# Performance work log

Measured on AMD Instinct MI355X. Metric: run time of the kernel, lower is better.

## Reference

```python
import jax, jax.numpy as jnp
import numpy as np

N_CELLS = 100000
IN_CH = 64
N_EDGES = 1280000


def setup_inputs() -> dict:
    key = jax.random.key(0)
    k1, k2, k3, k4, k5 = jax.random.split(key, 5)
    x_source = jax.random.normal(k1, (N_CELLS, IN_CH), dtype=jnp.float32)
    att_weight = jax.random.normal(k2, (2 * IN_CH,), dtype=jnp.float32)
    nbhd_values = jax.random.uniform(k3, (N_EDGES,), dtype=jnp.float32)
    target_index_i = jnp.sort(jax.random.randint(k4, (N_EDGES,), 0, N_CELLS))
    source_index_j = jax.random.randint(k5, (N_EDGES,), 0, N_CELLS)
    return {
        "x_source": x_source,
        "att_weight": att_weight,
        "nbhd_values": nbhd_values,
        "target_index_i": target_index_i,
        "source_index_j": source_index_j,
    }


def reference(x_source, att_weight, nbhd_values, target_index_i, source_index_j):
    # gather per-message endpoint features: [E, C] each
    x_src_msg = x_source[source_index_j]
    x_tgt_msg = x_source[target_index_i]  # x_target is None -> use x_source
    # attention: elu(cat([src, tgt]) @ w) -> [E]
    att = jax.nn.elu(
        jnp.concatenate([x_src_msg, x_tgt_msg], axis=1) @ att_weight
    )
    # modulate sparse neighborhood values by attention, scale messages
    vals = nbhd_values * att  # [E]
    x_message = vals[:, None] * x_src_msg  # [E, C]
    # scatter-sum into target cells: [N, C]
    return jax.ops.segment_sum(x_message, target_index_i, num_segments=N_CELLS)
```

## Files before the change

kernel.cpp:

```cpp
#include <hip/hip_runtime.h>

#define N_CELLS 100000
#define IN_CH 64
#define N_EDGES 1280000
#define NSEG 4
#define MAXW 4

__device__ __forceinline__ unsigned short f32_to_bf16(float f) {
    unsigned u = __float_as_uint(f);
    u += 0x7FFFu + ((u >> 16) & 1u);
    return (unsigned short)(u >> 16);
}
__device__ __forceinline__ float bf16_to_f32(unsigned short h) {
    return __uint_as_float((unsigned)h << 16);
}

#define SCORE_BLOCKS ((N_CELLS * 16 + 255) / 256)
#define ROWSTART_BLOCKS ((N_EDGES + 255) / 256)

__global__ void __launch_bounds__(256) prep_kernel(
    const float* __restrict__ x, const float* __restrict__ w,
    const int* __restrict__ tgt,
    float* __restrict__ s_src, float* __restrict__ s_tgt,
    unsigned short* __restrict__ xb, int* __restrict__ row_start,
    int n_cells, int n_edges) {
    if (blockIdx.x < SCORE_BLOCKS) {
        int gid  = blockIdx.x * 256 + threadIdx.x;
        int wave = gid >> 6;
        int lane = threadIdx.x & 63;
        int grp  = lane >> 4;
        int sub  = lane & 15;
        int cell = wave * 4 + grp;

        float4 xv = make_float4(0.f, 0.f, 0.f, 0.f);
        if (cell < n_cells)
            xv = *(const float4*)&x[(((unsigned)cell << 6) | ((unsigned)sub << 2))];
        if (xb && cell < n_cells) {
            ushort4 hb;
            hb.x = f32_to_bf16(xv.x); hb.y = f32_to_bf16(xv.y);
            hb.z = f32_to_bf16(xv.z); hb.w = f32_to_bf16(xv.w);
            *(ushort4*)&xb[(((unsigned)cell << 6) | ((unsigned)sub << 2))] = hb;
        }
        const float4* w4 = (const float4*)w;
        float4 wa = w4[sub];
        float4 wb = w4[16 + sub];
        float a = xv.x * wa.x + xv.y * wa.y + xv.z * wa.z + xv.w * wa.w;
        float b = xv.x * wb.x + xv.y * wb.y + xv.z * wb.z + xv.w * wb.w;
#pragma unroll
        for (int off = 8; off; off >>= 1) {
            a += __shfl_xor(a, off, 64);
            b += __shfl_xor(b, off, 64);
        }
        if (sub == 0 && cell < n_cells) {
            s_src[cell] = a;
            s_tgt[cell] = b;
        }
    } else {
        int e = (blockIdx.x - SCORE_BLOCKS) * 256 + threadIdx.x;
        if (e >= n_edges) return;
        int lane = threadIdx.x & 63;
        int t = tgt[e];
        int prev = __shfl_up(t, 1, 64);
        if (lane == 0) prev = (e == 0) ? -1 : tgt[e - 1];
        for (int c = prev + 1; c <= t; ++c) row_start[c] = e;
        if (e == n_edges - 1) {
            for (int c = t + 1; c <= n_cells; ++c) row_start[c] = n_edges;
        }
    }
}

__global__ void __launch_bounds__(256) agg_kernel_seg(
    const unsigned short* __restrict__ xb, const int* __restrict__ src,
    const float* __restrict__ nbhd,
    const float* __restrict__ s_src, const float* __restrict__ s_tgt,
    const int* __restrict__ row_start,
    float* __restrict__ out, int n_cells) {
    int gid  = blockIdx.x * blockDim.x + threadIdx.x;
    int lane = threadIdx.x & 63;
    int grp  = lane >> 4;
    int sub  = lane & 15;
    int cell = (gid >> 6) * 4 + grp;
    unsigned suboff = (unsigned)sub << 2;
    int gbase = grp << 4;

    int lo  = row_start[cell];
    int hi  = row_start[cell + 1];
    float sti = s_tgt[cell];
    int cnt  = hi - lo;
    int cntP = cnt > (MAXW * 16) ? (MAXW * 16) : cnt;

    const int q = (N_CELLS + NSEG - 1) / NSEG;

    int      jr[MAXW];
    float    vr[MAXW];
    unsigned bb[MAXW];

#pragma unroll
    for (int c = 0; c < MAXW; ++c) {
        int wcnt = cntP - (c << 4);
        wcnt = wcnt < 0 ? 0 : (wcnt > 16 ? 16 : wcnt);
        bool act = sub < wcnt;
        int j = 0; float v = 0.f;
        if (act) {
            int idx = lo + (c << 4) + sub;
            j = src[idx];
            float a = s_src[j] + sti;
            v = nbhd[idx] * (a > 0.f ? a : expm1f(a));
        }
        int b = act ? ((j >= 3 * q) ? 3 : (j >= 2 * q) ? 2 : (j >= q) ? 1 : 0) : 4;
        unsigned long long m0 = __ballot(b == 0);
        unsigned long long m1 = __ballot(b == 1);
        unsigned long long m2 = __ballot(b == 2);
        unsigned long long m3 = __ballot(b == 3);
        unsigned f0 = (unsigned)(m0 >> gbase) & 0xFFFFu;
        unsigned f1 = (unsigned)(m1 >> gbase) & 0xFFFFu;
        unsigned f2 = (unsigned)(m2 >> gbase) & 0xFFFFu;
        unsigned f3 = (unsigned)(m3 >> gbase) & 0xFFFFu;
        unsigned below = (1u << sub) - 1u;
        int c0 = __popc(f0), c1 = __popc(f1), c2 = __popc(f2), c3 = __popc(f3);
        int slot;
        if (b == 0)      slot = __popc(f0 & below);
        else if (b == 1) slot = c0 + __popc(f1 & below);
        else if (b == 2) slot = c0 + c1 + __popc(f2 & below);
        else if (b == 3) slot = c0 + c1 + c2 + __popc(f3 & below);
        else {
            unsigned f4 = ~(f0 | f1 | f2 | f3) & 0xFFFFu;
            slot = c0 + c1 + c2 + c3 + __popc(f4 & below);
        }
        int dst = (gbase + slot) << 2;
        jr[c] = __builtin_amdgcn_ds_permute(dst, j);
        vr[c] = __int_as_float(__builtin_amdgcn_ds_permute(dst, __float_as_int(v)));
        bb[c] = (unsigned)c0 | ((unsigned)(c0 + c1) << 5)
              | ((unsigned)(c0 + c1 + c2) << 10)
              | ((unsigned)(c0 + c1 + c2 + c3) << 15);
    }

    float4 acc = make_float4(0.f, 0.f, 0.f, 0.f);
#pragma unroll
    for (int s = 0; s < NSEG; ++s) {
#pragma unroll
        for (int c = 0; c < MAXW; ++c) {
            int t0 = (s == 0) ? 0 : (int)((bb[c] >> (5 * (s - 1))) & 31u);
            int t1 = (int)((bb[c] >> (5 * s)) & 31u);
            int t = t0;
            for (; t + 4 <= t1; t += 4) {
                int   j0 = __shfl(jr[c], gbase + t,     64);
                int   j1 = __shfl(jr[c], gbase + t + 1, 64);
                int   j2 = __shfl(jr[c], gbase + t + 2, 64);
                int   j3 = __shfl(jr[c], gbase + t + 3, 64);
                float v0 = __shfl(vr[c], gbase + t,     64);
                float v1 = __shfl(vr[c], gbase + t + 1, 64);
                float v2 = __shfl(vr[c], gbase + t + 2, 64);
                float v3 = __shfl(vr[c], gbase + t + 3, 64);
                ushort4 h0 = *(const ushort4*)&xb[(((unsigned)j0 << 6) | suboff)];
                ushort4 h1 = *(const ushort4*)&xb[(((unsigned)j1 << 6) | suboff)];
                ushort4 h2 = *(const ushort4*)&xb[(((unsigned)j2 << 6) | suboff)];
                ushort4 h3 = *(const ushort4*)&xb[(((unsigned)j3 << 6) | suboff)];
                acc.x = fmaf(v0, bf16_to_f32(h0.x), acc.x);
                acc.y = fmaf(v0, bf16_to_f32(h0.y), acc.y);
                acc.z = fmaf(v0, bf16_to_f32(h0.z), acc.z);
                acc.w = fmaf(v0, bf16_to_f32(h0.w), acc.w);
                acc.x = fmaf(v1, bf16_to_f32(h1.x), acc.x);
                acc.y = fmaf(v1, bf16_to_f32(h1.y), acc.y);
                acc.z = fmaf(v1, bf16_to_f32(h1.z), acc.z);
                acc.w = fmaf(v1, bf16_to_f32(h1.w), acc.w);
                acc.x = fmaf(v2, bf16_to_f32(h2.x), acc.x);
                acc.y = fmaf(v2, bf16_to_f32(h2.y), acc.y);
                acc.z = fmaf(v2, bf16_to_f32(h2.z), acc.z);
                acc.w = fmaf(v2, bf16_to_f32(h2.w), acc.w);
                acc.x = fmaf(v3, bf16_to_f32(h3.x), acc.x);
                acc.y = fmaf(v3, bf16_to_f32(h3.y), acc.y);
                acc.z = fmaf(v3, bf16_to_f32(h3.z), acc.z);
                acc.w = fmaf(v3, bf16_to_f32(h3.w), acc.w);
            }
            for (; t < t1; ++t) {
                int   jt = __shfl(jr[c], gbase + t, 64);
                float vt = __shfl(vr[c], gbase + t, 64);
                ushort4 h = *(const ushort4*)&xb[(((unsigned)jt << 6) | suboff)];
                acc.x = fmaf(vt, bf16_to_f32(h.x), acc.x);
                acc.y = fmaf(vt, bf16_to_f32(h.y), acc.y);
                acc.z = fmaf(vt, bf16_to_f32(h.z), acc.z);
                acc.w = fmaf(vt, bf16_to_f32(h.w), acc.w);
            }
        }
        if (s < NSEG - 1) __syncthreads();
    }

    for (int base = lo + MAXW * 16; base < hi; base += 16) {
        int cc = hi - base;
        if (cc > 16) cc = 16;
        int   j = 0;
        float v = 0.f;
        if (sub < cc) {
            j = src[base + sub];
            float a = s_src[j] + sti;
            v = nbhd[base + sub] * (a > 0.f ? a : expm1f(a));
        }
        for (int t = 0; t < cc; ++t) {
            int   jt = __shfl(j, gbase + t, 64);
            float vt = __shfl(v, gbase + t, 64);
            ushort4 h = *(const ushort4*)&xb[(((unsigned)jt << 6) | suboff)];
            acc.x = fmaf(vt, bf16_to_f32(h.x), acc.x);
            acc.y = fmaf(vt, bf16_to_f32(h.y), acc.y);
            acc.z = fmaf(vt, bf16_to_f32(h.z), acc.z);
            acc.w = fmaf(vt, bf16_to_f32(h.w), acc.w);
        }
    }

    *(float4*)&out[(((unsigned)cell << 6) | suboff)] = acc;
}

__global__ void __launch_bounds__(256) agg_kernel_f32(
    const float* __restrict__ x, const int* __restrict__ src,
    const float* __restrict__ nbhd,
    const float* __restrict__ s_src, const float* __restrict__ s_tgt,
    const int* __restrict__ row_start,
    float* __restrict__ out, int n_cells) {
    int gid  = blockIdx.x * blockDim.x + threadIdx.x;
    int lane = threadIdx.x & 63;
    int grp  = lane >> 4;
    int sub  = lane & 15;
    int cell = (gid >> 6) * 4 + grp;
    unsigned suboff = (unsigned)sub << 2;
    int gbase = grp << 4;

    int lo = 0, hi = 0;
    float sti = 0.f;
    if (cell < n_cells) {
        lo  = row_start[cell];
        hi  = row_start[cell + 1];
        sti = s_tgt[cell];
    }
    float4 acc = make_float4(0.f, 0.f, 0.f, 0.f);
    for (int base = lo; base < hi; base += 16) {
        int cc = hi - base;
        if (cc > 16) cc = 16;
        int   j = 0;
        float v = 0.f;
        if (sub < cc) {
            j = src[base + sub];
            float a = s_src[j] + sti;
            v = nbhd[base + sub] * (a > 0.f ? a : expm1f(a));
        }
        for (int t = 0; t < cc; ++t) {
            int   jt = __shfl(j, gbase + t, 64);
            float vt = __shfl(v, gbase + t, 64);
            float4 xt = *(const float4*)&x[(((unsigned)jt << 6) | suboff)];
            acc.x = fmaf(vt, xt.x, acc.x); acc.y = fmaf(vt, xt.y, acc.y);
            acc.z = fmaf(vt, xt.z, acc.z); acc.w = fmaf(vt, xt.w, acc.w);
        }
    }
    if (cell < n_cells)
        *(float4*)&out[(((unsigned)cell << 6) | suboff)] = acc;
}

extern "C" void kernel_launch(void* const* d_in, const int* in_sizes, int n_in,
                              void* d_out, int out_size, void* d_ws, size_t ws_size,
                              hipStream_t stream) {
    const float* x    = (const float*)d_in[0];
    const float* w    = (const float*)d_in[1];
    const float* nbhd = (const float*)d_in[2];
    const int*   tgt  = (const int*)d_in[3];
    const int*   src  = (const int*)d_in[4];
    float*       out  = (float*)d_out;

    float* s_src     = (float*)d_ws;
    float* s_tgt     = s_src + N_CELLS;
    int*   row_start = (int*)(s_tgt + N_CELLS);
    unsigned short* xb = (unsigned short*)(row_start + N_CELLS + 1);
    size_t need_bf16 = (size_t)(2 * N_CELLS + N_CELLS + 1) * 4 + (size_t)N_CELLS * IN_CH * 2;
    bool use_bf16 = ws_size >= need_bf16;

    if (use_bf16) {
        int blocks = SCORE_BLOCKS + ROWSTART_BLOCKS;
        prep_kernel<<<blocks, 256, 0, stream>>>(x, w, tgt, s_src, s_tgt, xb,
                                                row_start, N_CELLS, N_EDGES);
        int ablocks = (N_CELLS * 16) / 256;
        agg_kernel_seg<<<ablocks, 256, 0, stream>>>(xb, src, nbhd, s_src, s_tgt,
                                                    row_start, out, N_CELLS);
    } else {
        int blocks = SCORE_BLOCKS + ROWSTART_BLOCKS;
        prep_kernel<<<blocks, 256, 0, stream>>>(x, w, tgt, s_src, s_tgt,
                                                (unsigned short*)nullptr,
                                                row_start, N_CELLS, N_EDGES);
        int threads = 256;
        int ablocks = (N_CELLS * 16 + threads - 1) / threads;
        agg_kernel_f32<<<ablocks, threads, 0, stream>>>(x, src, nbhd, s_src, s_tgt,
                                                        row_start, out, N_CELLS);
    }
}
```

Measured before the change: 67.89 us.

## Precompute per-edge attention values in separate edge kernel, drop source-range bucketing

Splits the prep kernel into a score kernel and an edge kernel. The edge kernel computes each edge's elu-modulated weight once, stores it in a workspace array, and builds the row-start table. The aggregation kernel then only loads src and the precomputed value, with no s_src gather or expm1. It also drops the four-way source-range bucketing with ballots, permutes and block barriers in favour of a simple unrolled-by-8 gather loop. This adds a third launch, a dependency between score and edge kernels, and an extra write and read of the per-edge value array, and it gives up whatever locality the bucketing provided.

```diff
diff --git a/kernel.cpp b/kernel.cpp
--- a/kernel.cpp
+++ b/kernel.cpp
@@ -3,7 +3,6 @@
 #define N_CELLS 100000
 #define IN_CH 64
 #define N_EDGES 1280000
-#define NSEG 4
 #define MAXW 4
 
 __device__ __forceinline__ unsigned short f32_to_bf16(float f) {
@@ -15,67 +14,67 @@
     return __uint_as_float((unsigned)h << 16);
 }
 
-#define SCORE_BLOCKS ((N_CELLS * 16 + 255) / 256)
-#define ROWSTART_BLOCKS ((N_EDGES + 255) / 256)
-
-__global__ void __launch_bounds__(256) prep_kernel(
+__global__ void __launch_bounds__(256) score_kernel(
     const float* __restrict__ x, const float* __restrict__ w,
-    const int* __restrict__ tgt,
     float* __restrict__ s_src, float* __restrict__ s_tgt,
-    unsigned short* __restrict__ xb, int* __restrict__ row_start,
-    int n_cells, int n_edges) {
-    if (blockIdx.x < SCORE_BLOCKS) {
-        int gid  = blockIdx.x * 256 + threadIdx.x;
-        int wave = gid >> 6;
-        int lane = threadIdx.x & 63;
-        int grp  = lane >> 4;
-        int sub  = lane & 15;
-        int cell = wave * 4 + grp;
-
-        float4 xv = make_float4(0.f, 0.f, 0.f, 0.f);
-        if (cell < n_cells)
-            xv = *(const float4*)&x[(((unsigned)cell << 6) | ((unsigned)sub << 2))];
-        if (xb && cell < n_cells) {
-            ushort4 hb;
-            hb.x = f32_to_bf16(xv.x); hb.y = f32_to_bf16(xv.y);
-            hb.z = f32_to_bf16(xv.z); hb.w = f32_to_bf16(xv.w);
-            *(ushort4*)&xb[(((unsigned)cell << 6) | ((unsigned)sub << 2))] = hb;
-        }
-        const float4* w4 = (const float4*)w;
-        float4 wa = w4[sub];
-        float4 wb = w4[16 + sub];
-        float a = xv.x * wa.x + xv.y * wa.y + xv.z * wa.z + xv.w * wa.w;
-        float b = xv.x * wb.x + xv.y * wb.y + xv.z * wb.z + xv.w * wb.w;
-#pragma unroll
-        for (int off = 8; off; off >>= 1) {
-            a += __shfl_xor(a, off, 64);
-            b += __shfl_xor(b, off, 64);
-        }
-        if (sub == 0 && cell < n_cells) {
-            s_src[cell] = a;
-            s_tgt[cell] = b;
-        }
-    } else {
-        int e = (blockIdx.x - SCORE_BLOCKS) * 256 + threadIdx.x;
-        if (e >= n_edges) return;
-        int lane = threadIdx.x & 63;
-        int t = tgt[e];
-        int prev = __shfl_up(t, 1, 64);
-        if (lane == 0) prev = (e == 0) ? -1 : tgt[e - 1];
-        for (int c = prev + 1; c <= t; ++c) row_start[c] = e;
-        if (e == n_edges - 1) {
-            for (int c = t + 1; c <= n_cells; ++c) row_start[c] = n_edges;
-        }
-    }
-}
-
-__global__ void __launch_bounds__(256) agg_kernel_seg(
-    const unsigned short* __restrict__ xb, const int* __restrict__ src,
+    unsigned short* __restrict__ xb, int n_cells) {
+    int gid  = blockIdx.x * 256 + threadIdx.x;
+    int wave = gid >> 6;
+    int lane = threadIdx.x & 63;
+    int grp  = lane >> 4;
+    int sub  = lane & 15;
+    int cell = wave * 4 + grp;
+
+    float4 xv = make_float4(0.f, 0.f, 0.f, 0.f);
+    if (cell < n_cells)
+        xv = *(const float4*)&x[(((unsigned)cell << 6) | ((unsigned)sub << 2))];
+    if (xb && cell < n_cells) {
+        ushort4 hb;
+        hb.x = f32_to_bf16(xv.x); hb.y = f32_to_bf16(xv.y);
+        hb.z = f32_to_bf16(xv.z); hb.w = f32_to_bf16(xv.w);
+        *(ushort4*)&xb[(((unsigned)cell << 6) | ((unsigned)sub << 2))] = hb;
+    }
+    const float4* w4 = (const float4*)w;
+    float4 wa = w4[sub];
+    float4 wb = w4[16 + sub];
+    float a = xv.x * wa.x + xv.y * wa.y + xv.z * wa.z + xv.w * wa.w;
+    float b = xv.x * wb.x + xv.y * wb.y + xv.z * wb.z + xv.w * wb.w;
+#pragma unroll
+    for (int off = 8; off; off >>= 1) {
+        a += __shfl_xor(a, off, 64);
+        b += __shfl_xor(b, off, 64);
+    }
+    if (sub == 0 && cell < n_cells) {
+        s_src[cell] = a;
+        s_tgt[cell] = b;
+    }
+}
+
+__global__ void __launch_bounds__(256) edge_kernel(
+    const int* __restrict__ tgt, const int* __restrict__ src,
     const float* __restrict__ nbhd,
     const float* __restrict__ s_src, const float* __restrict__ s_tgt,
-    const int* __restrict__ row_start,
+    int* __restrict__ row_start, float* __restrict__ vals,
+    int n_edges, int n_cells) {
+    int e = blockIdx.x * 256 + threadIdx.x;
+    if (e >= n_edges) return;
+    int lane = threadIdx.x & 63;
+    int t = tgt[e];
+    float a = s_src[src[e]] + s_tgt[t];
+    vals[e] = nbhd[e] * (a > 0.f ? a : expm1f(a));
+    int prev = __shfl_up(t, 1, 64);
+    if (lane == 0) prev = (e == 0) ? -1 : tgt[e - 1];
+    for (int c = prev + 1; c <= t; ++c) row_start[c] = e;
+    if (e == n_edges - 1) {
+        for (int c = t + 1; c <= n_cells; ++c) row_start[c] = n_edges;
+    }
+}
+
+__global__ void __launch_bounds__(256) agg_kernel(
+    const unsigned short* __restrict__ xb, const int* __restrict__ src,
+    const float* __restrict__ vals, const int* __restrict__ row_start,
     float* __restrict__ out, int n_cells) {
-    int gid  = blockIdx.x * blockDim.x + threadIdx.x;
+    int gid  = blockIdx.x * 256 + threadIdx.x;
     int lane = threadIdx.x & 63;
     int grp  = lane >> 4;
     int sub  = lane & 15;
@@ -85,73 +84,41 @@
 
     int lo  = row_start[cell];
     int hi  = row_start[cell + 1];
-    float sti = s_tgt[cell];
-    int cnt  = hi - lo;
+    int cnt = hi - lo;
     int cntP = cnt > (MAXW * 16) ? (MAXW * 16) : cnt;
 
-    const int q = (N_CELLS + NSEG - 1) / NSEG;
-
-    int      jr[MAXW];
-    float    vr[MAXW];
-    unsigned bb[MAXW];
-
+    int   jr[MAXW];
+    float vr[MAXW];
 #pragma unroll
     for (int c = 0; c < MAXW; ++c) {
-        int wcnt = cntP - (c << 4);
-        wcnt = wcnt < 0 ? 0 : (wcnt > 16 ? 16 : wcnt);
-        bool act = sub < wcnt;
+        int t16 = (c << 4) + sub;
         int j = 0; float v = 0.f;
-        if (act) {
-            int idx = lo + (c << 4) + sub;
+        if (t16 < cntP) {
+            int idx = lo + t16;
             j = src[idx];
-            float a = s_src[j] + sti;
-            v = nbhd[idx] * (a > 0.f ? a : expm1f(a));
-        }
-        int b = act ? ((j >= 3 * q) ? 3 : (j >= 2 * q) ? 2 : (j >= q) ? 1 : 0) : 4;
-        unsigned long long m0 = __ballot(b == 0);
-        unsigned long long m1 = __ballot(b == 1);
-        unsigned long long m2 = __ballot(b == 2);
-        unsigned long long m3 = __ballot(b == 3);
-        unsigned f0 = (unsigned)(m0 >> gbase) & 0xFFFFu;
-        unsigned f1 = (unsigned)(m1 >> gbase) & 0xFFFFu;
-        unsigned f2 = (unsigned)(m2 >> gbase) & 0xFFFFu;
-        unsigned f3 = (unsigned)(m3 >> gbase) & 0xFFFFu;
-        unsigned below = (1u << sub) - 1u;
-        int c0 = __popc(f0), c1 = __popc(f1), c2 = __popc(f2), c3 = __popc(f3);
-        int slot;
-        if (b == 0)      slot = __popc(f0 & below);
-        else if (b == 1) slot = c0 + __popc(f1 & below);
-        else if (b == 2) slot = c0 + c1 + __popc(f2 & below);
-        else if (b == 3) slot = c0 + c1 + c2 + __popc(f3 & below);
-        else {
-            unsigned f4 = ~(f0 | f1 | f2 | f3) & 0xFFFFu;
-            slot = c0 + c1 + c2 + c3 + __popc(f4 & below);
-        }
-        int dst = (gbase + slot) << 2;
-        jr[c] = __builtin_amdgcn_ds_permute(dst, j);
-        vr[c] = __int_as_float(__builtin_amdgcn_ds_permute(dst, __float_as_int(v)));
-        bb[c] = (unsigned)c0 | ((unsigned)(c0 + c1) << 5)
-              | ((unsigned)(c0 + c1 + c2) << 10)
-              | ((unsigned)(c0 + c1 + c2 + c3) << 15);
+            v = vals[idx];
+        }
+        jr[c] = j; vr[c] = v;
     }
 
     float4 acc = make_float4(0.f, 0.f, 0.f, 0.f);
 #pragma unroll
-    for (int s = 0; s < NSEG; ++s) {
-#pragma unroll
-        for (int c = 0; c < MAXW; ++c) {
-            int t0 = (s == 0) ? 0 : (int)((bb[c] >> (5 * (s - 1))) & 31u);
-            int t1 = (int)((bb[c] >> (5 * s)) & 31u);
-            int t = t0;
-            for (; t + 4 <= t1; t += 4) {
-                int   j0 = __shfl(jr[c], gbase + t,     64);
-                int   j1 = __shfl(jr[c], gbase + t + 1, 64);
-                int   j2 = __shfl(jr[c], gbase + t + 2, 64);
-                int   j3 = __shfl(jr[c], gbase + t + 3, 64);
-                float v0 = __shfl(vr[c], gbase + t,     64);
-                float v1 = __shfl(vr[c], gbase + t + 1, 64);
-                float v2 = __shfl(vr[c], gbase + t + 2, 64);
-                float v3 = __shfl(vr[c], gbase + t + 3, 64);
+    for (int c = 0; c < MAXW; ++c) {
+        int wc = cntP - (c << 4);
+        if (wc <= 0) break;
+        if (wc > 16) wc = 16;
+        int t = 0;
+        for (; t + 8 <= wc; t += 8) {
+#pragma unroll
+            for (int u = 0; u < 8; u += 4) {
+                int   j0 = __shfl(jr[c], gbase + t + u,     64);
+                int   j1 = __shfl(jr[c], gbase + t + u + 1, 64);
+                int   j2 = __shfl(jr[c], gbase + t + u + 2, 64);
+                int   j3 = __shfl(jr[c], gbase + t + u + 3, 64);
+                float v0 = __shfl(vr[c], gbase + t + u,     64);
+                float v1 = __shfl(vr[c], gbase + t + u + 1, 64);
+                float v2 = __shfl(vr[c], gbase + t + u + 2, 64);
+                float v3 = __shfl(vr[c], gbase + t + u + 3, 64);
                 ushort4 h0 = *(const ushort4*)&xb[(((unsigned)j0 << 6) | suboff)];
                 ushort4 h1 = *(const ushort4*)&xb[(((unsigned)j1 << 6) | suboff)];
                 ushort4 h2 = *(const ushort4*)&xb[(((unsigned)j2 << 6) | suboff)];
@@ -173,17 +140,46 @@
                 acc.z = fmaf(v3, bf16_to_f32(h3.z), acc.z);
                 acc.w = fmaf(v3, bf16_to_f32(h3.w), acc.w);
             }
-            for (; t < t1; ++t) {
-                int   jt = __shfl(jr[c], gbase + t, 64);
-                float vt = __shfl(vr[c], gbase + t, 64);
-                ushort4 h = *(const ushort4*)&xb[(((unsigned)jt << 6) | suboff)];
-                acc.x = fmaf(vt, bf16_to_f32(h.x), acc.x);
-                acc.y = fmaf(vt, bf16_to_f32(h.y), acc.y);
-                acc.z = fmaf(vt, bf16_to_f32(h.z), acc.z);
-                acc.w = fmaf(vt, bf16_to_f32(h.w), acc.w);
-            }
-        }
-        if (s < NSEG - 1) __syncthreads();
+        }
+        for (; t + 4 <= wc; t += 4) {
+            int   j0 = __shfl(jr[c], gbase + t,     64);
+            int   j1 = __shfl(jr[c], gbase + t + 1, 64);
+            int   j2 = __shfl(jr[c], gbase + t + 2, 64);
+            int   j3 = __shfl(jr[c], gbase + t + 3, 64);
+            float v0 = __shfl(vr[c], gbase + t,     64);
+            float v1 = __shfl(vr[c], gbase + t + 1, 64);
+            float v2 = __shfl(vr[c], gbase + t + 2, 64);
+            float v3 = __shfl(vr[c], gbase + t + 3, 64);
+            ushort4 h0 = *(const ushort4*)&xb[(((unsigned)j0 << 6) | suboff)];
+            ushort4 h1 = *(const ushort4*)&xb[(((unsigned)j1 << 6) | suboff)];
+            ushort4 h2 = *(const ushort4*)&xb[(((unsigned)j2 << 6) | suboff)];
+            ushort4 h3 = *(const ushort4*)&xb[(((unsigned)j3 << 6) | suboff)];
+            acc.x = fmaf(v0, bf16_to_f32(h0.x), acc.x);
+            acc.y = fmaf(v0, bf16_to_f32(h0.y), acc.y);
+            acc.z = fmaf(v0, bf16_to_f32(h0.z), acc.z);
+            acc.w = fmaf(v0, bf16_to_f32(h0.w), acc.w);
+            acc.x = fmaf(v1, bf16_to_f32(h1.x), acc.x);
+            acc.y = fmaf(v1, bf16_to_f32(h1.y), acc.y);
+            acc.z = fmaf(v1, bf16_to_f32(h1.z), acc.z);
+            acc.w = fmaf(v1, bf16_to_f32(h1.w), acc.w);
+            acc.x = fmaf(v2, bf16_to_f32(h2.x), acc.x);
+            acc.y = fmaf(v2, bf16_to_f32(h2.y), acc.y);
+            acc.z = fmaf(v2, bf16_to_f32(h2.z), acc.z);
+            acc.w = fmaf(v2, bf16_to_f32(h2.w), acc.w);
+            acc.x = fmaf(v3, bf16_to_f32(h3.x), acc.x);
+            acc.y = fmaf(v3, bf16_to_f32(h3.y), acc.y);
+            acc.z = fmaf(v3, bf16_to_f32(h3.z), acc.z);
+            acc.w = fmaf(v3, bf16_to_f32(h3.w), acc.w);
+        }
+        for (; t < wc; ++t) {
+            int   jt = __shfl(jr[c], gbase + t, 64);
+            float vt = __shfl(vr[c], gbase + t, 64);
+            ushort4 h = *(const ushort4*)&xb[(((unsigned)jt << 6) | suboff)];
+            acc.x = fmaf(vt, bf16_to_f32(h.x), acc.x);
+            acc.y = fmaf(vt, bf16_to_f32(h.y), acc.y);
+            acc.z = fmaf(vt, bf16_to_f32(h.z), acc.z);
+            acc.w = fmaf(vt, bf16_to_f32(h.w), acc.w);
+        }
     }
 
     for (int base = lo + MAXW * 16; base < hi; base += 16) {
@@ -193,8 +189,7 @@
         float v = 0.f;
         if (sub < cc) {
             j = src[base + sub];
-            float a = s_src[j] + sti;
-            v = nbhd[base + sub] * (a > 0.f ? a : expm1f(a));
+            v = vals[base + sub];
         }
         for (int t = 0; t < cc; ++t) {
             int   jt = __shfl(j, gbase + t, 64);
@@ -216,7 +211,7 @@
     const float* __restrict__ s_src, const float* __restrict__ s_tgt,
     const int* __restrict__ row_start,
     float* __restrict__ out, int n_cells) {
-    int gid  = blockIdx.x * blockDim.x + threadIdx.x;
+    int gid  = blockIdx.x * 256 + threadIdx.x;
     int lane = threadIdx.x & 63;
     int grp  = lane >> 4;
     int sub  = lane & 15;
@@ -267,25 +262,28 @@
     float* s_src     = (float*)d_ws;
     float* s_tgt     = s_src + N_CELLS;
     int*   row_start = (int*)(s_tgt + N_CELLS);
-    unsigned short* xb = (unsigned short*)(row_start + N_CELLS + 1);
-    size_t need_bf16 = (size_t)(2 * N_CELLS + N_CELLS + 1) * 4 + (size_t)N_CELLS * IN_CH * 2;
-    bool use_bf16 = ws_size >= need_bf16;
-
-    if (use_bf16) {
-        int blocks = SCORE_BLOCKS + ROWSTART_BLOCKS;
-        prep_kernel<<<blocks, 256, 0, stream>>>(x, w, tgt, s_src, s_tgt, xb,
-                                                row_start, N_CELLS, N_EDGES);
+    float* vals      = (float*)(row_start + N_CELLS + 1);
+    unsigned short* xb = (unsigned short*)(vals + N_EDGES);
+    size_t need_full = (size_t)(3 * N_CELLS + 1 + N_EDGES) * 4
+                     + (size_t)N_CELLS * IN_CH * 2;
+    bool full = ws_size >= need_full;
+
+    int sblocks = (N_CELLS * 16 + 255) / 256;
+    int eblocks = (N_EDGES + 255) / 256;
+
+    if (full) {
+        score_kernel<<<sblocks, 256, 0, stream>>>(x, w, s_src, s_tgt, xb, N_CELLS);
+        edge_kernel<<<eblocks, 256, 0, stream>>>(tgt, src, nbhd, s_src, s_tgt,
+                                                 row_start, vals, N_EDGES, N_CELLS);
         int ablocks = (N_CELLS * 16) / 256;
-        agg_kernel_seg<<<ablocks, 256, 0, stream>>>(xb, src, nbhd, s_src, s_tgt,
+        agg_kernel<<<ablocks, 256, 0, stream>>>(xb, src, vals, row_start, out, N_CELLS);
+    } else {
+        score_kernel<<<sblocks, 256, 0, stream>>>(x, w, s_src, s_tgt,
+                                                  (unsigned short*)nullptr, N_CELLS);
+        edge_kernel<<<eblocks, 256, 0, stream>>>(tgt, src, nbhd, s_src, s_tgt,
+                                                 row_start, vals, N_EDGES, N_CELLS);
+        int ablocks = (N_CELLS * 16 + 255) / 256;
+        agg_kernel_f32<<<ablocks, 256, 0, stream>>>(x, src, nbhd, s_src, s_tgt,
                                                     row_start, out, N_CELLS);
-    } else {
-        int blocks = SCORE_BLOCKS + ROWSTART_BLOCKS;
-        prep_kernel<<<blocks, 256, 0, stream>>>(x, w, tgt, s_src, s_tgt,
-                                                (unsigned short*)nullptr,
-                                                row_start, N_CELLS, N_EDGES);
-        int threads = 256;
-        int ablocks = (N_CELLS * 16 + threads - 1) / threads;
-        agg_kernel_f32<<<ablocks, threads, 0, stream>>>(x, src, nbhd, s_src, s_tgt,
-                                                        row_start, out, N_CELLS);
-    }
-}
+    }
+}
```

Result: faster. 64.71 us (-4.7%).
